# Performance work log

Hardware: AMD Instinct MI355X
Metric: run time of the kernel (lower is better)

The kernel has to match this reference:

```python
import jax, jax.numpy as jnp
import numpy as np

N, D = 262144, 64
L, K = 4, 1024


def setup_inputs() -> dict:
    key = jax.random.key(0)
    k1, k2 = jax.random.split(key)
    features = jax.random.normal(k1, (N, D), dtype=jnp.float32)
    codebooks = jax.random.normal(k2, (L, K, D), dtype=jnp.float32)
    return {"features": features, "codebooks": codebooks}


def reference(features, codebooks):
    """Residual VQ: per level, nearest-center (L2) argmin, gather, subtract.

    Uses squared distances (same argmin as torch.cdist p=2).
    """

    def step(residuals, centers):
        # ||r - c||^2 = ||r||^2 - 2 r.c + ||c||^2   -> [N, K]
        d = (
            jnp.sum(residuals * residuals, axis=1, keepdims=True)
            - 2.0 * (residuals @ centers.T)
            + jnp.sum(centers * centers, axis=1)
        )
        idx = jnp.argmin(d, axis=1)          # [N] int32
        quantized = centers[idx]             # [N, D] gather
        return residuals - quantized, (quantized, idx)

    _, (quantized_levels, indices) = jax.lax.scan(step, features, codebooks)
    quantized_result = jnp.sum(quantized_levels, axis=0)  # sum over L levels
    return quantized_result, indices  # indices: [L, N]
```

## Files before the change

kernel.cpp:

```cpp
#include <hip/hip_runtime.h>
#include <math.h>

constexpr int RVQ_N = 262144;
constexpr int RVQ_D = 64;
constexpr int RVQ_L = 4;
constexpr int RVQ_K = 1024;

typedef __attribute__((ext_vector_type(8))) short short8;
typedef __attribute__((ext_vector_type(4))) float floatx4;

__device__ __forceinline__ unsigned short f2bf(float f) {
  unsigned int u = __float_as_uint(f);
  u += 0x7fffu + ((u >> 16) & 1u);
  return (unsigned short)(u >> 16);
}
__device__ __forceinline__ float bf2f(unsigned short h) {
  return __uint_as_float(((unsigned int)h) << 16);
}
__device__ __forceinline__ void split2(float x, unsigned short& h0,
                                       unsigned short& h1) {
  h0 = f2bf(x);
  float r1 = x - bf2f(h0);
  h1 = f2bf(r1);
}
__device__ __forceinline__ void load8(const float* p, float* v) {
  float4 a = *(const float4*)p;
  float4 b = *(const float4*)(p + 4);
  v[0] = a.x; v[1] = a.y; v[2] = a.z; v[3] = a.w;
  v[4] = b.x; v[5] = b.y; v[6] = b.z; v[7] = b.w;
}

__global__ __launch_bounds__(256) void rvq_prep_split(
    const float* __restrict__ cb, unsigned short* __restrict__ bh,
    unsigned short* __restrict__ bm) {
  int i = blockIdx.x * 256 + threadIdx.x;
  float c2 = -2.0f * cb[i];
  unsigned short h0, h1;
  split2(c2, h0, h1);
  bh[i] = h0;
  bm[i] = h1;
}

__global__ __launch_bounds__(256) void rvq_cnorm_kernel(
    const float* __restrict__ cb, float* __restrict__ cnorm,
    float* __restrict__ cnormB) {
  int i = blockIdx.x * blockDim.x + threadIdx.x;
  const float* c = cb + (size_t)i * RVQ_D;
  float a0 = 0.f, a1 = 0.f, a2 = 0.f, a3 = 0.f;
#pragma unroll
  for (int d = 0; d < RVQ_D; d += 4) {
    float4 v = *reinterpret_cast<const float4*>(c + d);
    a0 = fmaf(v.x, v.x, a0);
    a1 = fmaf(v.y, v.y, a1);
    a2 = fmaf(v.z, v.z, a2);
    a3 = fmaf(v.w, v.w, a3);
  }
  float s = (a0 + a1) + (a2 + a3);
  cnorm[i] = s;
  cnormB[i] = s + 256.0f;
}

__device__ __forceinline__ void load_bt(const unsigned short* __restrict__ bh,
                                        const unsigned short* __restrict__ bmp,
                                        const float* __restrict__ cnl, int nt,
                                        int m, int q, short8 (&b)[2][2],
                                        float& cc) {
  size_t rowoff = (size_t)(nt * 16 + m) * RVQ_D + q * 8;
  b[0][0] = *(const short8*)(bh + rowoff);
  b[0][1] = *(const short8*)(bh + rowoff + 32);
  b[1][0] = *(const short8*)(bmp + rowoff);
  b[1][1] = *(const short8*)(bmp + rowoff + 32);
  cc = cnl[nt * 16 + m];
}

__global__ __launch_bounds__(256, 3) void rvq_mfma_kernel(
    const float* __restrict__ feat, const float* __restrict__ cb,
    const unsigned short* __restrict__ cb_hi,
    const unsigned short* __restrict__ cb_mid,
    const float* __restrict__ cnorm, const float* __restrict__ cnormB,
    float* __restrict__ out_q, float* __restrict__ out_idx) {
  const int tid = threadIdx.x;
  const int lane = tid & 63;
  const int wave = tid >> 6;
  const int m = lane & 15;
  const int q = lane >> 4;
  const int base = blockIdx.x * 256 + wave * 64;
  const int g = base + lane;

  int ci0 = 0, ci1 = 0, ci2 = 0;

  constexpr int AC[3] = {0, 0, 1};
  constexpr int BC[3] = {0, 1, 0};

#pragma unroll
  for (int l = 0; l < RVQ_L; ++l) {
    const unsigned short* bh = cb_hi + (size_t)l * RVQ_K * RVQ_D;
    const unsigned short* bmp = cb_mid + (size_t)l * RVQ_K * RVQ_D;
    const float* cnBl = cnormB + (size_t)l * RVQ_K;
    const float* cnl = cnorm + (size_t)l * RVQ_K;
    const float* cbl = cb + (size_t)l * RVQ_K * RVQ_D;

    short8 afr[4][2][2];
#pragma unroll
    for (int t = 0; t < 4; ++t) {
      const int p = t * 16 + m;
      int j0 = 0, j1 = 0, j2 = 0;
      if (l > 0) j0 = __shfl(ci0, p);
      if (l > 1) j1 = __shfl(ci1, p);
      if (l > 2) j2 = __shfl(ci2, p);
      const float* fp = feat + (size_t)(base + p) * RVQ_D;
      const float* c0p = cb + (size_t)j0 * RVQ_D;
      const float* c1p = cb + ((size_t)RVQ_K + j1) * RVQ_D;
      const float* c2p = cb + ((size_t)2 * RVQ_K + j2) * RVQ_D;
#pragma unroll
      for (int oct = 0; oct < 2; ++oct) {
        const int dof = oct * 32 + q * 8;
        float v[8];
        load8(fp + dof, v);
        if (l > 0) {
          float c[8];
          load8(c0p + dof, c);
#pragma unroll
          for (int e = 0; e < 8; ++e) v[e] -= c[e];
        }
        if (l > 1) {
          float c[8];
          load8(c1p + dof, c);
#pragma unroll
          for (int e = 0; e < 8; ++e) v[e] -= c[e];
        }
        if (l > 2) {
          float c[8];
          load8(c2p + dof, c);
#pragma unroll
          for (int e = 0; e < 8; ++e) v[e] -= c[e];
        }
#pragma unroll
        for (int e = 0; e < 8; ++e) {
          unsigned short h0, h1;
          split2(v[e], h0, h1);
          afr[t][0][oct][e] = (short)h0;
          afr[t][1][oct][e] = (short)h1;
        }
      }
    }

    unsigned p1[4][4], p2[4][4];
#pragma unroll
    for (int t = 0; t < 4; ++t)
#pragma unroll
      for (int r2 = 0; r2 < 4; ++r2) {
        p1[t][r2] = 0xFFFFFFFFu;
        p2[t][r2] = 0xFFFFFFFFu;
      }

    short8 bA[2][2], bB[2][2];
    float ccA, ccB;
    load_bt(bh, bmp, cnBl, 0, m, q, bA, ccA);

    for (int nt = 0; nt < RVQ_K / 16; nt += 2) {
      load_bt(bh, bmp, cnBl, nt + 1, m, q, bB, ccB);
      {
        floatx4 acc[4];
#pragma unroll
        for (int t = 0; t < 4; ++t) {
          acc[t][0] = ccA; acc[t][1] = ccA; acc[t][2] = ccA; acc[t][3] = ccA;
        }
#pragma unroll
        for (int s = 0; s < 3; ++s)
#pragma unroll
          for (int oct = 0; oct < 2; ++oct)
#pragma unroll
            for (int t = 0; t < 4; ++t)
              acc[t] = __builtin_amdgcn_mfma_f32_16x16x32_bf16(
                  afr[t][AC[s]][oct], bA[BC[s]][oct], acc[t], 0, 0, 0);
        unsigned nbits = (unsigned)nt;
#pragma unroll
        for (int t = 0; t < 4; ++t)
#pragma unroll
          for (int r2 = 0; r2 < 4; ++r2) {
            unsigned u = (__float_as_uint(acc[t][r2]) & 0xFFFFFFC0u) | nbits;
            unsigned mx = p1[t][r2] > u ? p1[t][r2] : u;
            p1[t][r2] = p1[t][r2] < u ? p1[t][r2] : u;
            p2[t][r2] = p2[t][r2] < mx ? p2[t][r2] : mx;
          }
      }
      int ntn = (nt + 2 < RVQ_K / 16) ? nt + 2 : nt;
      load_bt(bh, bmp, cnBl, ntn, m, q, bA, ccA);
      {
        floatx4 acc[4];
#pragma unroll
        for (int t = 0; t < 4; ++t) {
          acc[t][0] = ccB; acc[t][1] = ccB; acc[t][2] = ccB; acc[t][3] = ccB;
        }
#pragma unroll
        for (int s = 0; s < 3; ++s)
#pragma unroll
          for (int oct = 0; oct < 2; ++oct)
#pragma unroll
            for (int t = 0; t < 4; ++t)
              acc[t] = __builtin_amdgcn_mfma_f32_16x16x32_bf16(
                  afr[t][AC[s]][oct], bB[BC[s]][oct], acc[t], 0, 0, 0);
        unsigned nbits = (unsigned)(nt + 1);
#pragma unroll
        for (int t = 0; t < 4; ++t)
#pragma unroll
          for (int r2 = 0; r2 < 4; ++r2) {
            unsigned u = (__float_as_uint(acc[t][r2]) & 0xFFFFFFC0u) | nbits;
            unsigned mx = p1[t][r2] > u ? p1[t][r2] : u;
            p1[t][r2] = p1[t][r2] < u ? p1[t][r2] : u;
            p2[t][r2] = p2[t][r2] < mx ? p2[t][r2] : mx;
          }
      }
    }

    int cand[4] = {0, 0, 0, 0};
    const int srcl = ((lane >> 2) & 3) << 4;
#pragma unroll
    for (int t = 0; t < 4; ++t)
#pragma unroll
      for (int r2 = 0; r2 < 4; ++r2) {
        unsigned a = p1[t][r2], b = p2[t][r2];
        int ka = (int)((a & 63u) << 4) | m;
        int kb = (int)((b & 63u) << 4) | m;
        unsigned va = (a & 0xFFFFFC00u) | (unsigned)ka;
        unsigned vb = (b & 0xFFFFFC00u) | (unsigned)kb;
        if (vb < va) { unsigned tu = va; va = vb; vb = tu; }
        int ck[4];
#pragma unroll
        for (int pass = 0; pass < 4; ++pass) {
          unsigned gm = va;
#pragma unroll
          for (int off = 1; off <= 8; off <<= 1) {
            unsigned o = (unsigned)__shfl_xor((int)gm, off);
            gm = gm < o ? gm : o;
          }
          ck[pass] = (int)(gm & 1023u);
          bool hit = (va == gm);
          va = hit ? vb : va;
          vb = hit ? 0xFFFFFFFFu : vb;
        }
        int v1 = __shfl(ck[0], srcl);
        int v2 = __shfl(ck[1], srcl);
        int v3 = __shfl(ck[2], srcl);
        int v4 = __shfl(ck[3], srcl);
        bool take = (q == t) && ((lane & 3) == r2);
        if (take) { cand[0] = v1; cand[1] = v2; cand[2] = v3; cand[3] = v4; }
      }

    {
      int tmp;
      if (cand[0] > cand[1]) { tmp = cand[0]; cand[0] = cand[1]; cand[1] = tmp; }
      if (cand[2] > cand[3]) { tmp = cand[2]; cand[2] = cand[3]; cand[3] = tmp; }
      if (cand[0] > cand[2]) { tmp = cand[0]; cand[0] = cand[2]; cand[2] = tmp; }
      if (cand[1] > cand[3]) { tmp = cand[1]; cand[1] = cand[3]; cand[3] = tmp; }
      if (cand[1] > cand[2]) { tmp = cand[1]; cand[1] = cand[2]; cand[2] = tmp; }
    }

    float r_[RVQ_D];
    {
      const float4* f4p = (const float4*)(feat + (size_t)g * RVQ_D);
#pragma unroll
      for (int i = 0; i < 16; ++i) {
        float4 v = f4p[i];
        r_[4 * i + 0] = v.x; r_[4 * i + 1] = v.y;
        r_[4 * i + 2] = v.z; r_[4 * i + 3] = v.w;
      }
      if (l > 0) {
        const float4* cp = (const float4*)(cb + (size_t)ci0 * RVQ_D);
#pragma unroll
        for (int i = 0; i < 16; ++i) {
          float4 v = cp[i];
          r_[4 * i + 0] -= v.x; r_[4 * i + 1] -= v.y;
          r_[4 * i + 2] -= v.z; r_[4 * i + 3] -= v.w;
        }
      }
      if (l > 1) {
        const float4* cp = (const float4*)(cb + ((size_t)RVQ_K + ci1) * RVQ_D);
#pragma unroll
        for (int i = 0; i < 16; ++i) {
          float4 v = cp[i];
          r_[4 * i + 0] -= v.x; r_[4 * i + 1] -= v.y;
          r_[4 * i + 2] -= v.z; r_[4 * i + 3] -= v.w;
        }
      }
      if (l > 2) {
        const float4* cp =
            (const float4*)(cb + ((size_t)2 * RVQ_K + ci2) * RVQ_D);
#pragma unroll
        for (int i = 0; i < 16; ++i) {
          float4 v = cp[i];
          r_[4 * i + 0] -= v.x; r_[4 * i + 1] -= v.y;
          r_[4 * i + 2] -= v.z; r_[4 * i + 3] -= v.w;
        }
      }
    }

    float s0 = 0.f, s1 = 0.f, s2 = 0.f, s3 = 0.f;
#pragma unroll
    for (int i = 0; i < 16; ++i) {
      s0 = fmaf(r_[4 * i + 0], r_[4 * i + 0], s0);
      s1 = fmaf(r_[4 * i + 1], r_[4 * i + 1], s1);
      s2 = fmaf(r_[4 * i + 2], r_[4 * i + 2], s2);
      s3 = fmaf(r_[4 * i + 3], r_[4 * i + 3], s3);
    }
    const float rr = (s0 + s1) + (s2 + s3);

    float best = INFINITY;
    int ci = 0;
#pragma unroll
    for (int jc = 0; jc < 4; ++jc) {
      int k = cand[jc];
      const float4* c4 = (const float4*)(cbl + (size_t)k * RVQ_D);
      float a0 = 0.f, a1 = 0.f, a2 = 0.f, a3 = 0.f;
#pragma unroll
      for (int i = 0; i < 16; ++i) {
        float4 v = c4[i];
        a0 = fmaf(r_[4 * i + 0], v.x, a0);
        a1 = fmaf(r_[4 * i + 1], v.y, a1);
        a2 = fmaf(r_[4 * i + 2], v.z, a2);
        a3 = fmaf(r_[4 * i + 3], v.w, a3);
      }
      float dot = (a0 + a1) + (a2 + a3);
      float score = (rr - 2.0f * dot) + cnl[k];
      if (score < best) {
        best = score;
        ci = k;
      }
    }

    if (l == 0) ci0 = ci;
    else if (l == 1) ci1 = ci;
    else if (l == 2) ci2 = ci;

    if (l == RVQ_L - 1) {
      const float4* crow = (const float4*)(cbl + (size_t)ci * RVQ_D);
      const float4* f4p = (const float4*)(feat + (size_t)g * RVQ_D);
      float4* o4 = (float4*)(out_q + (size_t)g * RVQ_D);
#pragma unroll
      for (int i = 0; i < 16; ++i) {
        float4 cv = crow[i];
        float4 fv = f4p[i];
        float rn0 = r_[4 * i + 0] - cv.x;
        float rn1 = r_[4 * i + 1] - cv.y;
        float rn2 = r_[4 * i + 2] - cv.z;
        float rn3 = r_[4 * i + 3] - cv.w;
        float4 o;
        o.x = fv.x - rn0;
        o.y = fv.y - rn1;
        o.z = fv.z - rn2;
        o.w = fv.w - rn3;
        o4[i] = o;
      }
    }
    out_idx[(size_t)l * RVQ_N + g] = (float)ci;
  }
}

extern "C" void kernel_launch(void* const* d_in, const int* in_sizes, int n_in,
                              void* d_out, int out_size, void* d_ws,
                              size_t ws_size, hipStream_t stream) {
  const float* features = (const float*)d_in[0];
  const float* codebooks = (const float*)d_in[1];
  float* out_q = (float*)d_out;
  float* out_idx = (float*)d_out + (size_t)RVQ_N * RVQ_D;

  const size_t comp_elems = (size_t)RVQ_L * RVQ_K * RVQ_D;
  unsigned short* cb_hi = (unsigned short*)d_ws;
  unsigned short* cb_mid = cb_hi + comp_elems;
  float* cnorm = (float*)(cb_mid + comp_elems);
  float* cnormB = cnorm + (size_t)RVQ_L * RVQ_K;

  hipLaunchKernelGGL(rvq_prep_split, dim3(comp_elems / 256), dim3(256), 0,
                     stream, codebooks, cb_hi, cb_mid);
  hipLaunchKernelGGL(rvq_cnorm_kernel, dim3((RVQ_L * RVQ_K) / 256), dim3(256),
                     0, stream, codebooks, cnorm, cnormB);
  hipLaunchKernelGGL(rvq_mfma_kernel, dim3(RVQ_N / 256), dim3(256), 0, stream,
                     features, codebooks, cb_hi, cb_mid, cnorm, cnormB, out_q,
                     out_idx);
}
```

Baseline: 979.5 us.

## Split 4-tile MFMA sweep into two 2-tile passes, use med3 for top-2

```diff
diff --git a/kernel.cpp b/kernel.cpp
--- a/kernel.cpp
+++ b/kernel.cpp
@@ -28,6 +28,12 @@
   float4 b = *(const float4*)(p + 4);
   v[0] = a.x; v[1] = a.y; v[2] = a.z; v[3] = a.w;
   v[4] = b.x; v[5] = b.y; v[6] = b.z; v[7] = b.w;
+}
+
+__device__ __forceinline__ unsigned med3u(unsigned a, unsigned b, unsigned c) {
+  unsigned d;
+  asm("v_med3_u32 %0, %1, %2, %3" : "=v"(d) : "v"(a), "v"(b), "v"(c));
+  return d;
 }
 
 __global__ __launch_bounds__(256) void rvq_prep_split(
@@ -73,7 +79,7 @@
   cc = cnl[nt * 16 + m];
 }
 
-__global__ __launch_bounds__(256, 3) void rvq_mfma_kernel(
+__global__ __launch_bounds__(256, 4) void rvq_mfma_kernel(
     const float* __restrict__ feat, const float* __restrict__ cb,
     const unsigned short* __restrict__ cb_hi,
     const unsigned short* __restrict__ cb_mid,
@@ -100,153 +106,162 @@
     const float* cnl = cnorm + (size_t)l * RVQ_K;
     const float* cbl = cb + (size_t)l * RVQ_K * RVQ_D;
 
-    short8 afr[4][2][2];
-#pragma unroll
-    for (int t = 0; t < 4; ++t) {
-      const int p = t * 16 + m;
-      int j0 = 0, j1 = 0, j2 = 0;
-      if (l > 0) j0 = __shfl(ci0, p);
-      if (l > 1) j1 = __shfl(ci1, p);
-      if (l > 2) j2 = __shfl(ci2, p);
-      const float* fp = feat + (size_t)(base + p) * RVQ_D;
-      const float* c0p = cb + (size_t)j0 * RVQ_D;
-      const float* c1p = cb + ((size_t)RVQ_K + j1) * RVQ_D;
-      const float* c2p = cb + ((size_t)2 * RVQ_K + j2) * RVQ_D;
-#pragma unroll
-      for (int oct = 0; oct < 2; ++oct) {
-        const int dof = oct * 32 + q * 8;
-        float v[8];
-        load8(fp + dof, v);
-        if (l > 0) {
-          float c[8];
-          load8(c0p + dof, c);
-#pragma unroll
-          for (int e = 0; e < 8; ++e) v[e] -= c[e];
-        }
-        if (l > 1) {
-          float c[8];
-          load8(c1p + dof, c);
-#pragma unroll
-          for (int e = 0; e < 8; ++e) v[e] -= c[e];
-        }
-        if (l > 2) {
-          float c[8];
-          load8(c2p + dof, c);
-#pragma unroll
-          for (int e = 0; e < 8; ++e) v[e] -= c[e];
-        }
-#pragma unroll
-        for (int e = 0; e < 8; ++e) {
-          unsigned short h0, h1;
-          split2(v[e], h0, h1);
-          afr[t][0][oct][e] = (short)h0;
-          afr[t][1][oct][e] = (short)h1;
-        }
-      }
-    }
-
-    unsigned p1[4][4], p2[4][4];
-#pragma unroll
-    for (int t = 0; t < 4; ++t)
-#pragma unroll
-      for (int r2 = 0; r2 < 4; ++r2) {
-        p1[t][r2] = 0xFFFFFFFFu;
-        p2[t][r2] = 0xFFFFFFFFu;
-      }
-
-    short8 bA[2][2], bB[2][2];
-    float ccA, ccB;
-    load_bt(bh, bmp, cnBl, 0, m, q, bA, ccA);
-
-    for (int nt = 0; nt < RVQ_K / 16; nt += 2) {
-      load_bt(bh, bmp, cnBl, nt + 1, m, q, bB, ccB);
-      {
-        floatx4 acc[4];
-#pragma unroll
-        for (int t = 0; t < 4; ++t) {
-          acc[t][0] = ccA; acc[t][1] = ccA; acc[t][2] = ccA; acc[t][3] = ccA;
-        }
-#pragma unroll
-        for (int s = 0; s < 3; ++s)
-#pragma unroll
-          for (int oct = 0; oct < 2; ++oct)
-#pragma unroll
-            for (int t = 0; t < 4; ++t)
-              acc[t] = __builtin_amdgcn_mfma_f32_16x16x32_bf16(
-                  afr[t][AC[s]][oct], bA[BC[s]][oct], acc[t], 0, 0, 0);
-        unsigned nbits = (unsigned)nt;
-#pragma unroll
-        for (int t = 0; t < 4; ++t)
-#pragma unroll
-          for (int r2 = 0; r2 < 4; ++r2) {
-            unsigned u = (__float_as_uint(acc[t][r2]) & 0xFFFFFFC0u) | nbits;
-            unsigned mx = p1[t][r2] > u ? p1[t][r2] : u;
-            p1[t][r2] = p1[t][r2] < u ? p1[t][r2] : u;
-            p2[t][r2] = p2[t][r2] < mx ? p2[t][r2] : mx;
-          }
-      }
-      int ntn = (nt + 2 < RVQ_K / 16) ? nt + 2 : nt;
-      load_bt(bh, bmp, cnBl, ntn, m, q, bA, ccA);
-      {
-        floatx4 acc[4];
-#pragma unroll
-        for (int t = 0; t < 4; ++t) {
-          acc[t][0] = ccB; acc[t][1] = ccB; acc[t][2] = ccB; acc[t][3] = ccB;
-        }
-#pragma unroll
-        for (int s = 0; s < 3; ++s)
-#pragma unroll
-          for (int oct = 0; oct < 2; ++oct)
-#pragma unroll
-            for (int t = 0; t < 4; ++t)
-              acc[t] = __builtin_amdgcn_mfma_f32_16x16x32_bf16(
-                  afr[t][AC[s]][oct], bB[BC[s]][oct], acc[t], 0, 0, 0);
-        unsigned nbits = (unsigned)(nt + 1);
-#pragma unroll
-        for (int t = 0; t < 4; ++t)
-#pragma unroll
-          for (int r2 = 0; r2 < 4; ++r2) {
-            unsigned u = (__float_as_uint(acc[t][r2]) & 0xFFFFFFC0u) | nbits;
-            unsigned mx = p1[t][r2] > u ? p1[t][r2] : u;
-            p1[t][r2] = p1[t][r2] < u ? p1[t][r2] : u;
-            p2[t][r2] = p2[t][r2] < mx ? p2[t][r2] : mx;
-          }
-      }
-    }
-
     int cand[4] = {0, 0, 0, 0};
-    const int srcl = ((lane >> 2) & 3) << 4;
-#pragma unroll
-    for (int t = 0; t < 4; ++t)
-#pragma unroll
-      for (int r2 = 0; r2 < 4; ++r2) {
-        unsigned a = p1[t][r2], b = p2[t][r2];
-        int ka = (int)((a & 63u) << 4) | m;
-        int kb = (int)((b & 63u) << 4) | m;
-        unsigned va = (a & 0xFFFFFC00u) | (unsigned)ka;
-        unsigned vb = (b & 0xFFFFFC00u) | (unsigned)kb;
-        if (vb < va) { unsigned tu = va; va = vb; vb = tu; }
-        int ck[4];
-#pragma unroll
-        for (int pass = 0; pass < 4; ++pass) {
-          unsigned gm = va;
-#pragma unroll
-          for (int off = 1; off <= 8; off <<= 1) {
-            unsigned o = (unsigned)__shfl_xor((int)gm, off);
-            gm = gm < o ? gm : o;
-          }
-          ck[pass] = (int)(gm & 1023u);
-          bool hit = (va == gm);
-          va = hit ? vb : va;
-          vb = hit ? 0xFFFFFFFFu : vb;
-        }
-        int v1 = __shfl(ck[0], srcl);
-        int v2 = __shfl(ck[1], srcl);
-        int v3 = __shfl(ck[2], srcl);
-        int v4 = __shfl(ck[3], srcl);
-        bool take = (q == t) && ((lane & 3) == r2);
-        if (take) { cand[0] = v1; cand[1] = v2; cand[2] = v3; cand[3] = v4; }
-      }
+
+#pragma unroll
+    for (int pass = 0; pass < 2; ++pass) {
+      short8 afr[2][2][2];
+#pragma unroll
+      for (int tl = 0; tl < 2; ++tl) {
+        const int t = pass * 2 + tl;
+        const int p = t * 16 + m;
+        int j0 = 0, j1 = 0, j2 = 0;
+        if (l > 0) j0 = __shfl(ci0, p);
+        if (l > 1) j1 = __shfl(ci1, p);
+        if (l > 2) j2 = __shfl(ci2, p);
+        const float* fp = feat + (size_t)(base + p) * RVQ_D;
+        const float* c0p = cb + (size_t)j0 * RVQ_D;
+        const float* c1p = cb + ((size_t)RVQ_K + j1) * RVQ_D;
+        const float* c2p = cb + ((size_t)2 * RVQ_K + j2) * RVQ_D;
+#pragma unroll
+        for (int oct = 0; oct < 2; ++oct) {
+          const int dof = oct * 32 + q * 8;
+          float v[8];
+          load8(fp + dof, v);
+          if (l > 0) {
+            float c[8];
+            load8(c0p + dof, c);
+#pragma unroll
+            for (int e = 0; e < 8; ++e) v[e] -= c[e];
+          }
+          if (l > 1) {
+            float c[8];
+            load8(c1p + dof, c);
+#pragma unroll
+            for (int e = 0; e < 8; ++e) v[e] -= c[e];
+          }
+          if (l > 2) {
+            float c[8];
+            load8(c2p + dof, c);
+#pragma unroll
+            for (int e = 0; e < 8; ++e) v[e] -= c[e];
+          }
+#pragma unroll
+          for (int e = 0; e < 8; ++e) {
+            unsigned short h0, h1;
+            split2(v[e], h0, h1);
+            afr[tl][0][oct][e] = (short)h0;
+            afr[tl][1][oct][e] = (short)h1;
+          }
+        }
+      }
+
+      unsigned p1[2][4], p2[2][4];
+#pragma unroll
+      for (int tl = 0; tl < 2; ++tl)
+#pragma unroll
+        for (int r2 = 0; r2 < 4; ++r2) {
+          p1[tl][r2] = 0xFFFFFFFFu;
+          p2[tl][r2] = 0xFFFFFFFFu;
+        }
+
+      short8 bA[2][2], bB[2][2];
+      float ccA, ccB;
+      load_bt(bh, bmp, cnBl, 0, m, q, bA, ccA);
+
+      for (int nt = 0; nt < RVQ_K / 16; nt += 2) {
+        load_bt(bh, bmp, cnBl, nt + 1, m, q, bB, ccB);
+        {
+          floatx4 acc[2];
+#pragma unroll
+          for (int tl = 0; tl < 2; ++tl) {
+            acc[tl][0] = ccA; acc[tl][1] = ccA;
+            acc[tl][2] = ccA; acc[tl][3] = ccA;
+          }
+#pragma unroll
+          for (int s = 0; s < 3; ++s)
+#pragma unroll
+            for (int oct = 0; oct < 2; ++oct)
+#pragma unroll
+              for (int tl = 0; tl < 2; ++tl)
+                acc[tl] = __builtin_amdgcn_mfma_f32_16x16x32_bf16(
+                    afr[tl][AC[s]][oct], bA[BC[s]][oct], acc[tl], 0, 0, 0);
+          unsigned nbits = (unsigned)nt;
+#pragma unroll
+          for (int tl = 0; tl < 2; ++tl)
+#pragma unroll
+            for (int r2 = 0; r2 < 4; ++r2) {
+              unsigned u =
+                  (__float_as_uint(acc[tl][r2]) & 0xFFFFFFC0u) | nbits;
+              p2[tl][r2] = med3u(p1[tl][r2], p2[tl][r2], u);
+              p1[tl][r2] = p1[tl][r2] < u ? p1[tl][r2] : u;
+            }
+        }
+        int ntn = (nt + 2 < RVQ_K / 16) ? nt + 2 : nt;
+        load_bt(bh, bmp, cnBl, ntn, m, q, bA, ccA);
+        {
+          floatx4 acc[2];
+#pragma unroll
+          for (int tl = 0; tl < 2; ++tl) {
+            acc[tl][0] = ccB; acc[tl][1] = ccB;
+            acc[tl][2] = ccB; acc[tl][3] = ccB;
+          }
+#pragma unroll
+          for (int s = 0; s < 3; ++s)
+#pragma unroll
+            for (int oct = 0; oct < 2; ++oct)
+#pragma unroll
+              for (int tl = 0; tl < 2; ++tl)
+                acc[tl] = __builtin_amdgcn_mfma_f32_16x16x32_bf16(
+                    afr[tl][AC[s]][oct], bB[BC[s]][oct], acc[tl], 0, 0, 0);
+          unsigned nbits = (unsigned)(nt + 1);
+#pragma unroll
+          for (int tl = 0; tl < 2; ++tl)
+#pragma unroll
+            for (int r2 = 0; r2 < 4; ++r2) {
+              unsigned u =
+                  (__float_as_uint(acc[tl][r2]) & 0xFFFFFFC0u) | nbits;
+              p2[tl][r2] = med3u(p1[tl][r2], p2[tl][r2], u);
+              p1[tl][r2] = p1[tl][r2] < u ? p1[tl][r2] : u;
+            }
+        }
+      }
+
+      const int srcl = ((lane >> 2) & 3) << 4;
+#pragma unroll
+      for (int tl = 0; tl < 2; ++tl) {
+        const int t = pass * 2 + tl;
+#pragma unroll
+        for (int r2 = 0; r2 < 4; ++r2) {
+          unsigned a = p1[tl][r2], b = p2[tl][r2];
+          int ka = (int)((a & 63u) << 4) | m;
+          int kb = (int)((b & 63u) << 4) | m;
+          unsigned va = (a & 0xFFFFFC00u) | (unsigned)ka;
+          unsigned vb = (b & 0xFFFFFC00u) | (unsigned)kb;
+          if (vb < va) { unsigned tu = va; va = vb; vb = tu; }
+          int ck[4];
+#pragma unroll
+          for (int pss = 0; pss < 4; ++pss) {
+            unsigned gm = va;
+#pragma unroll
+            for (int off = 1; off <= 8; off <<= 1) {
+              unsigned o = (unsigned)__shfl_xor((int)gm, off);
+              gm = gm < o ? gm : o;
+            }
+            ck[pss] = (int)(gm & 1023u);
+            bool hit = (va == gm);
+            va = hit ? vb : va;
+            vb = hit ? 0xFFFFFFFFu : vb;
+          }
+          int v1 = __shfl(ck[0], srcl);
+          int v2 = __shfl(ck[1], srcl);
+          int v3 = __shfl(ck[2], srcl);
+          int v4 = __shfl(ck[3], srcl);
+          bool take = (q == t) && ((lane & 3) == r2);
+          if (take) { cand[0] = v1; cand[1] = v2; cand[2] = v3; cand[3] = v4; }
+        }
+      }
+    }
 
     {
       int tmp;
```

Measured after the change: 1.519 ms. 1.55x slower.
